# Kernel optimization log

Hardware: AMD Instinct MI355X
Metric: run time of the kernel (lower is better)

The kernel has to match this reference:

```python
import jax, jax.numpy as jnp
import numpy as np

B, N, F_IN, F_OUT = 128, 512, 128, 64
ALPHA = 0.2        # LeakyReLU slope for attention logits
GAIN = 1.414       # xavier gain used in the torch module
NEG_INF = -9e15    # mask value from the torch code


def _xavier_uniform(key, shape, gain):
    fan_in, fan_out = shape[0], shape[1]
    limit = gain * np.sqrt(6.0 / (fan_in + fan_out))
    return jax.random.uniform(key, shape, jnp.float32, -limit, limit)


def setup_inputs() -> dict:
    key = jax.random.key(0)
    k1, k2, k3, k4 = jax.random.split(key, 4)
    input_hid = jax.random.normal(k1, (B, N, F_IN), jnp.float32)
    adj = jax.random.randint(k2, (B, N, N), 0, 2, jnp.int32)  # 0/1 adjacency
    W = _xavier_uniform(k3, (F_IN, F_OUT), GAIN)
    a = _xavier_uniform(k4, (2 * F_OUT, 1), GAIN)
    return {"input_hid": input_hid, "adj": adj, "W": W, "a": a}


def reference(input_hid, adj, W, a):
    # h: [B, N, F_OUT]
    h = jnp.matmul(input_hid, W)
    # Standard GAT decomposition of the concat-repeat construction:
    # e[b,i,j] = leakyrelu( [h_i || h_j] @ a ) = leakyrelu( h_i@a_src + h_j@a_dst )
    a_src = a[:F_OUT, 0]   # applies to the repeated-row (i) half
    a_dst = a[F_OUT:, 0]   # applies to the tiled (j) half
    s = jnp.einsum('bnf,f->bn', h, a_src)  # [B, N]
    t = jnp.einsum('bnf,f->bn', h, a_dst)  # [B, N]
    e = jax.nn.leaky_relu(s[:, :, None] + t[:, None, :], ALPHA)  # [B, N, N]
    e = jnp.where(adj > 0, e, NEG_INF)
    att = jax.nn.softmax(e, axis=2)        # softmax over neighbors j
    h_prime = jnp.matmul(att, h)           # [B, N, F_OUT]
    # concat=True -> F.leaky_relu with torch default slope 0.01
    return jax.nn.leaky_relu(h_prime, 0.01)
```

## Files before the change

kernel.cpp:

```cpp
#include <hip/hip_runtime.h>
#include <stdint.h>

#define B_   128
#define N_   512
#define FIN  128
#define FOUT 64

using bf16x8 = __attribute__((ext_vector_type(8))) short;
using f32x4  = __attribute__((ext_vector_type(4))) float;

__device__ inline unsigned short f2bf(float x) {
    union { float f; uint32_t u; } c; c.f = x;
    uint32_t u = c.u;
    return (unsigned short)((u + 0x7FFFu + ((u >> 16) & 1u)) >> 16);
}

__global__ __launch_bounds__(256) void k_h(const float* __restrict__ X,
                                           const float* __restrict__ W,
                                           const float* __restrict__ a,
                                           uint16_t* __restrict__ htT,
                                           float* __restrict__ s,
                                           float* __restrict__ t) {
    __shared__ bf16x8 ax[32 * 64];
    __shared__ bf16x8 wl[16 * 64];

    const int b  = blockIdx.x >> 2;
    const int j0 = (blockIdx.x & 3) * 128;
    const int tid = threadIdx.x;
    const int w = tid >> 6, lane = tid & 63;
    const int q = lane >> 4, m = lane & 15;

#pragma unroll
    for (int nt = 0; nt < 4; ++nt) {
        bf16x8 fr;
#pragma unroll
        for (int u = 0; u < 8; ++u)
            fr[u] = (short)f2bf(W[(w * 32 + q * 8 + u) * FOUT + nt * 16 + m]);
        wl[(w * 4 + nt) * 64 + lane] = fr;
    }

    const float* xb = X + ((size_t)(b * N_) + j0) * FIN;
#pragma unroll
    for (int i = 0; i < 8; ++i) {
        int pi = i * 4 + w, rt = pi >> 2, ks = pi & 3;
        const float* src = xb + (size_t)(rt * 16 + m) * FIN + ks * 32 + q * 8;
        float4 v0 = *(const float4*)src;
        float4 v1 = *(const float4*)(src + 4);
        bf16x8 fr;
        fr[0] = (short)f2bf(v0.x); fr[1] = (short)f2bf(v0.y);
        fr[2] = (short)f2bf(v0.z); fr[3] = (short)f2bf(v0.w);
        fr[4] = (short)f2bf(v1.x); fr[5] = (short)f2bf(v1.y);
        fr[6] = (short)f2bf(v1.z); fr[7] = (short)f2bf(v1.w);
        ax[pi * 64 + lane] = fr;
    }
    __syncthreads();

    float asv[4], adv[4];
#pragma unroll
    for (int nt = 0; nt < 4; ++nt) {
        asv[nt] = a[nt * 16 + m];
        adv[nt] = a[FOUT + nt * 16 + m];
    }

    for (int rl = 0; rl < 2; ++rl) {
        const int rt = w + rl * 4;
        f32x4 acc[4] = {{0.f,0.f,0.f,0.f},{0.f,0.f,0.f,0.f},
                        {0.f,0.f,0.f,0.f},{0.f,0.f,0.f,0.f}};
#pragma unroll
        for (int ks = 0; ks < 4; ++ks) {
            bf16x8 af = ax[(rt * 4 + ks) * 64 + lane];
#pragma unroll
            for (int nt = 0; nt < 4; ++nt)
                acc[nt] = __builtin_amdgcn_mfma_f32_16x16x32_bf16(
                    af, wl[(ks * 4 + nt) * 64 + lane], acc[nt], 0, 0, 0);
        }

        float ps[4], pt[4];
#pragma unroll
        for (int r = 0; r < 4; ++r) {
            float vs = 0.f, vt = 0.f;
#pragma unroll
            for (int nt = 0; nt < 4; ++nt) {
                vs += acc[nt][r] * asv[nt];
                vt += acc[nt][r] * adv[nt];
            }
            vs += __shfl_xor(vs, 1, 64); vs += __shfl_xor(vs, 2, 64);
            vs += __shfl_xor(vs, 4, 64); vs += __shfl_xor(vs, 8, 64);
            vt += __shfl_xor(vt, 1, 64); vt += __shfl_xor(vt, 2, 64);
            vt += __shfl_xor(vt, 4, 64); vt += __shfl_xor(vt, 8, 64);
            ps[r] = vs; pt[r] = vt;
        }
        if (m < 4) {
            float vs = (m == 0) ? ps[0] : (m == 1) ? ps[1] : (m == 2) ? ps[2] : ps[3];
            float vt = (m == 0) ? pt[0] : (m == 1) ? pt[1] : (m == 2) ? pt[2] : pt[3];
            int row = j0 + rt * 16 + q * 4 + m;
            s[b * N_ + row] = vs;
            t[b * N_ + row] = vt;
        }

#pragma unroll
        for (int nt = 0; nt < 4; ++nt) {
            uint32_t d0 = (uint32_t)f2bf(acc[nt][0]) | ((uint32_t)f2bf(acc[nt][1]) << 16);
            uint32_t d1 = (uint32_t)f2bf(acc[nt][2]) | ((uint32_t)f2bf(acc[nt][3]) << 16);
            uint2 dd; dd.x = d0; dd.y = d1;
            *(uint2*)(htT + (size_t)(b * FOUT + nt * 16 + m) * N_ + j0 + rt * 16 + q * 4) = dd;
        }
    }
}

__global__ __launch_bounds__(256) void k_attn(const int*    __restrict__ adj,
                                              const uint16_t* __restrict__ htT,
                                              const float*  __restrict__ s,
                                              const float*  __restrict__ t,
                                              float*        __restrict__ out) {
    __shared__ bf16x8 hstage[64 * 64];

    const int b  = blockIdx.x >> 2;
    const int i0 = (blockIdx.x & 3) * 128;
    const int tid = threadIdx.x;
    const int w = tid >> 6, lane = tid & 63;
    const int q = lane >> 4, m = lane & 15;

    const uint16_t* hb = htT + (size_t)b * FOUT * N_;
#pragma unroll
    for (int i = 0; i < 16; ++i) {
        int pi = i * 4 + w, ks = pi >> 2, nt = pi & 3;
        bf16x8 v = *(const bf16x8*)(hb + (size_t)(nt * 16 + m) * N_ + ks * 32 + q * 8);
        hstage[pi * 64 + lane] = v;
    }
    __syncthreads();

    const float* tb = t + b * N_;

    for (int rl = 0; rl < 2; ++rl) {
        const int rt = w + rl * 4;
        const int irow = i0 + rt * 16 + m;
        const float s_i = s[b * N_ + irow];
        const int* adjrow = adj + ((size_t)(b * N_) + irow) * N_;

        f32x4 acc0 = {0.f,0.f,0.f,0.f}, acc1 = {0.f,0.f,0.f,0.f};
        f32x4 acc2 = {0.f,0.f,0.f,0.f}, acc3 = {0.f,0.f,0.f,0.f};
        float lsum = 0.f;

        for (int ks = 0; ks < 16; ++ks) {
            const int jb = ks * 32 + q * 8;
            float4 t0 = *(const float4*)(tb + jb);
            float4 t1 = *(const float4*)(tb + jb + 4);
            int4  a0 = *(const int4*)(adjrow + jb);
            int4  a1 = *(const int4*)(adjrow + jb + 4);

            float tj[8] = {t0.x, t0.y, t0.z, t0.w, t1.x, t1.y, t1.z, t1.w};
            int   av[8] = {a0.x, a0.y, a0.z, a0.w, a1.x, a1.y, a1.z, a1.w};
            float pv[8];
#pragma unroll
            for (int u = 0; u < 8; ++u) {
                float e = s_i + tj[u];
                e = fmaxf(e, 0.2f * e);
                pv[u] = (av[u] > 0) ? __expf(e) : 0.0f;
                lsum += pv[u];
            }
            bf16x8 af;
#pragma unroll
            for (int u = 0; u < 8; ++u) af[u] = (short)f2bf(pv[u]);

            bf16x8 b0 = hstage[(ks * 4 + 0) * 64 + lane];
            bf16x8 b1 = hstage[(ks * 4 + 1) * 64 + lane];
            bf16x8 b2 = hstage[(ks * 4 + 2) * 64 + lane];
            bf16x8 b3 = hstage[(ks * 4 + 3) * 64 + lane];

            acc0 = __builtin_amdgcn_mfma_f32_16x16x32_bf16(af, b0, acc0, 0, 0, 0);
            acc1 = __builtin_amdgcn_mfma_f32_16x16x32_bf16(af, b1, acc1, 0, 0, 0);
            acc2 = __builtin_amdgcn_mfma_f32_16x16x32_bf16(af, b2, acc2, 0, 0, 0);
            acc3 = __builtin_amdgcn_mfma_f32_16x16x32_bf16(af, b3, acc3, 0, 0, 0);
        }

        lsum += __shfl_xor(lsum, 16, 64);
        lsum += __shfl_xor(lsum, 32, 64);

#pragma unroll
        for (int reg = 0; reg < 4; ++reg) {
            float lr = __shfl(lsum, q * 4 + reg, 64);
            float inv = 1.0f / lr;
            int orow = i0 + rt * 16 + q * 4 + reg;
            size_t obase = ((size_t)(b * N_) + orow) * FOUT + m;
            float v0 = acc0[reg] * inv; v0 = fmaxf(v0, 0.01f * v0);
            float v1 = acc1[reg] * inv; v1 = fmaxf(v1, 0.01f * v1);
            float v2 = acc2[reg] * inv; v2 = fmaxf(v2, 0.01f * v2);
            float v3 = acc3[reg] * inv; v3 = fmaxf(v3, 0.01f * v3);
            out[obase +  0] = v0;
            out[obase + 16] = v1;
            out[obase + 32] = v2;
            out[obase + 48] = v3;
        }
    }
}

extern "C" void kernel_launch(void* const* d_in, const int* in_sizes, int n_in,
                              void* d_out, int out_size, void* d_ws, size_t ws_size,
                              hipStream_t stream) {
    const float* X   = (const float*)d_in[0];
    const int*   adj = (const int*)  d_in[1];
    const float* W   = (const float*)d_in[2];
    const float* a   = (const float*)d_in[3];
    float* out = (float*)d_out;

    uint16_t* htT = (uint16_t*)d_ws;
    float* s = (float*)(htT + (size_t)B_ * FOUT * N_);
    float* t = s + B_ * N_;

    k_h<<<B_ * 4, 256, 0, stream>>>(X, W, a, htT, s, t);
    k_attn<<<B_ * 4, 256, 0, stream>>>(adj, htT, s, t, out);
}
```

Before: 232.3 us.

## Process both row tiles together, prefetch adjacency, stage t in LDS

The attention kernel now handles its two 16-row tiles in a single fused loop instead of two sequential passes. It software-prefetches the next adjacency chunk one iteration ahead and stages the t vector in shared memory rather than reloading it from global memory each step. The aim is more memory-level parallelism on the dominant adjacency stream and shared B-fragment loads across both tiles. The cost is higher register pressure from doubled accumulators and prefetch registers, which may reduce occupancy.

```diff
diff --git a/kernel.cpp b/kernel.cpp
--- a/kernel.cpp
+++ b/kernel.cpp
@@ -114,6 +114,7 @@
                                               const float*  __restrict__ t,
                                               float*        __restrict__ out) {
     __shared__ bf16x8 hstage[64 * 64];
+    __shared__ float  tsh[N_];
 
     const int b  = blockIdx.x >> 2;
     const int i0 = (blockIdx.x & 3) * 128;
@@ -128,69 +129,92 @@
         bf16x8 v = *(const bf16x8*)(hb + (size_t)(nt * 16 + m) * N_ + ks * 32 + q * 8);
         hstage[pi * 64 + lane] = v;
     }
+    *(float2*)&tsh[tid * 2] = *(const float2*)(t + b * N_ + tid * 2);
     __syncthreads();
 
-    const float* tb = t + b * N_;
-
-    for (int rl = 0; rl < 2; ++rl) {
-        const int rt = w + rl * 4;
-        const int irow = i0 + rt * 16 + m;
-        const float s_i = s[b * N_ + irow];
-        const int* adjrow = adj + ((size_t)(b * N_) + irow) * N_;
-
-        f32x4 acc0 = {0.f,0.f,0.f,0.f}, acc1 = {0.f,0.f,0.f,0.f};
-        f32x4 acc2 = {0.f,0.f,0.f,0.f}, acc3 = {0.f,0.f,0.f,0.f};
-        float lsum = 0.f;
-
-        for (int ks = 0; ks < 16; ++ks) {
-            const int jb = ks * 32 + q * 8;
-            float4 t0 = *(const float4*)(tb + jb);
-            float4 t1 = *(const float4*)(tb + jb + 4);
-            int4  a0 = *(const int4*)(adjrow + jb);
-            int4  a1 = *(const int4*)(adjrow + jb + 4);
-
-            float tj[8] = {t0.x, t0.y, t0.z, t0.w, t1.x, t1.y, t1.z, t1.w};
-            int   av[8] = {a0.x, a0.y, a0.z, a0.w, a1.x, a1.y, a1.z, a1.w};
-            float pv[8];
-#pragma unroll
-            for (int u = 0; u < 8; ++u) {
-                float e = s_i + tj[u];
-                e = fmaxf(e, 0.2f * e);
-                pv[u] = (av[u] > 0) ? __expf(e) : 0.0f;
-                lsum += pv[u];
-            }
-            bf16x8 af;
-#pragma unroll
-            for (int u = 0; u < 8; ++u) af[u] = (short)f2bf(pv[u]);
-
-            bf16x8 b0 = hstage[(ks * 4 + 0) * 64 + lane];
-            bf16x8 b1 = hstage[(ks * 4 + 1) * 64 + lane];
-            bf16x8 b2 = hstage[(ks * 4 + 2) * 64 + lane];
-            bf16x8 b3 = hstage[(ks * 4 + 3) * 64 + lane];
-
-            acc0 = __builtin_amdgcn_mfma_f32_16x16x32_bf16(af, b0, acc0, 0, 0, 0);
-            acc1 = __builtin_amdgcn_mfma_f32_16x16x32_bf16(af, b1, acc1, 0, 0, 0);
-            acc2 = __builtin_amdgcn_mfma_f32_16x16x32_bf16(af, b2, acc2, 0, 0, 0);
-            acc3 = __builtin_amdgcn_mfma_f32_16x16x32_bf16(af, b3, acc3, 0, 0, 0);
-        }
-
-        lsum += __shfl_xor(lsum, 16, 64);
-        lsum += __shfl_xor(lsum, 32, 64);
-
-#pragma unroll
-        for (int reg = 0; reg < 4; ++reg) {
-            float lr = __shfl(lsum, q * 4 + reg, 64);
-            float inv = 1.0f / lr;
-            int orow = i0 + rt * 16 + q * 4 + reg;
-            size_t obase = ((size_t)(b * N_) + orow) * FOUT + m;
-            float v0 = acc0[reg] * inv; v0 = fmaxf(v0, 0.01f * v0);
-            float v1 = acc1[reg] * inv; v1 = fmaxf(v1, 0.01f * v1);
-            float v2 = acc2[reg] * inv; v2 = fmaxf(v2, 0.01f * v2);
-            float v3 = acc3[reg] * inv; v3 = fmaxf(v3, 0.01f * v3);
-            out[obase +  0] = v0;
-            out[obase + 16] = v1;
-            out[obase + 32] = v2;
-            out[obase + 48] = v3;
+    const int ir0 = i0 + w * 16 + m;
+    const int ir1 = ir0 + 64;
+    const float s0 = s[b * N_ + ir0];
+    const float s1 = s[b * N_ + ir1];
+    const int* ar0 = adj + ((size_t)(b * N_) + ir0) * N_;
+    const int* ar1 = adj + ((size_t)(b * N_) + ir1) * N_;
+
+    f32x4 acc0[4] = {{0.f,0.f,0.f,0.f},{0.f,0.f,0.f,0.f},
+                     {0.f,0.f,0.f,0.f},{0.f,0.f,0.f,0.f}};
+    f32x4 acc1[4] = {{0.f,0.f,0.f,0.f},{0.f,0.f,0.f,0.f},
+                     {0.f,0.f,0.f,0.f},{0.f,0.f,0.f,0.f}};
+    float ls0 = 0.f, ls1 = 0.f;
+
+    int4 c00 = *(const int4*)(ar0 + q * 8);
+    int4 c01 = *(const int4*)(ar0 + q * 8 + 4);
+    int4 c10 = *(const int4*)(ar1 + q * 8);
+    int4 c11 = *(const int4*)(ar1 + q * 8 + 4);
+
+    for (int ks = 0; ks < 16; ++ks) {
+        const int jn = ((ks < 15) ? ks + 1 : ks) * 32 + q * 8;
+        int4 n00 = *(const int4*)(ar0 + jn);
+        int4 n01 = *(const int4*)(ar0 + jn + 4);
+        int4 n10 = *(const int4*)(ar1 + jn);
+        int4 n11 = *(const int4*)(ar1 + jn + 4);
+
+        const int jb = ks * 32 + q * 8;
+        float tj[8];
+#pragma unroll
+        for (int u = 0; u < 8; ++u) tj[u] = tsh[jb + u];
+
+        int av0[8] = {c00.x, c00.y, c00.z, c00.w, c01.x, c01.y, c01.z, c01.w};
+        int av1[8] = {c10.x, c10.y, c10.z, c10.w, c11.x, c11.y, c11.z, c11.w};
+        bf16x8 af0, af1;
+#pragma unroll
+        for (int u = 0; u < 8; ++u) {
+            float e0 = s0 + tj[u];
+            e0 = fmaxf(e0, 0.2f * e0);
+            float p0 = (av0[u] > 0) ? __expf(e0) : 0.0f;
+            ls0 += p0;
+            af0[u] = (short)f2bf(p0);
+            float e1 = s1 + tj[u];
+            e1 = fmaxf(e1, 0.2f * e1);
+            float p1 = (av1[u] > 0) ? __expf(e1) : 0.0f;
+            ls1 += p1;
+            af1[u] = (short)f2bf(p1);
+        }
+
+        bf16x8 bf0 = hstage[(ks * 4 + 0) * 64 + lane];
+        bf16x8 bf1 = hstage[(ks * 4 + 1) * 64 + lane];
+        bf16x8 bf2 = hstage[(ks * 4 + 2) * 64 + lane];
+        bf16x8 bf3 = hstage[(ks * 4 + 3) * 64 + lane];
+
+        acc0[0] = __builtin_amdgcn_mfma_f32_16x16x32_bf16(af0, bf0, acc0[0], 0, 0, 0);
+        acc0[1] = __builtin_amdgcn_mfma_f32_16x16x32_bf16(af0, bf1, acc0[1], 0, 0, 0);
+        acc0[2] = __builtin_amdgcn_mfma_f32_16x16x32_bf16(af0, bf2, acc0[2], 0, 0, 0);
+        acc0[3] = __builtin_amdgcn_mfma_f32_16x16x32_bf16(af0, bf3, acc0[3], 0, 0, 0);
+        acc1[0] = __builtin_amdgcn_mfma_f32_16x16x32_bf16(af1, bf0, acc1[0], 0, 0, 0);
+        acc1[1] = __builtin_amdgcn_mfma_f32_16x16x32_bf16(af1, bf1, acc1[1], 0, 0, 0);
+        acc1[2] = __builtin_amdgcn_mfma_f32_16x16x32_bf16(af1, bf2, acc1[2], 0, 0, 0);
+        acc1[3] = __builtin_amdgcn_mfma_f32_16x16x32_bf16(af1, bf3, acc1[3], 0, 0, 0);
+
+        c00 = n00; c01 = n01; c10 = n10; c11 = n11;
+    }
+
+    ls0 += __shfl_xor(ls0, 16, 64);
+    ls0 += __shfl_xor(ls0, 32, 64);
+    ls1 += __shfl_xor(ls1, 16, 64);
+    ls1 += __shfl_xor(ls1, 32, 64);
+
+#pragma unroll
+    for (int reg = 0; reg < 4; ++reg) {
+        float lr0 = __shfl(ls0, q * 4 + reg, 64);
+        float lr1 = __shfl(ls1, q * 4 + reg, 64);
+        float inv0 = 1.0f / lr0, inv1 = 1.0f / lr1;
+        int orow0 = i0 + w * 16 + q * 4 + reg;
+        size_t ob0 = ((size_t)(b * N_) + orow0) * FOUT + m;
+        size_t ob1 = ob0 + (size_t)64 * FOUT;
+#pragma unroll
+        for (int nt = 0; nt < 4; ++nt) {
+            float v0 = acc0[nt][reg] * inv0; v0 = fmaxf(v0, 0.01f * v0);
+            float v1 = acc1[nt][reg] * inv1; v1 = fmaxf(v1, 0.01f * v1);
+            out[ob0 + nt * 16] = v0;
+            out[ob1 + nt * 16] = v1;
         }
     }
 }
```

New measurement: 231.7 us. Within noise of the previous version (-0.3%).

## Shrink attention tiles, halve LDS staging, prefetch adjacency, load X directly

Applied to the files above, without the earlier changes.

The attention kernel now gives each block 64 rows instead of 128 and launches twice as many blocks. It stages the bf16 h matrix in two halves so LDS drops to half, caches t in shared memory, and prefetches the next adjacency chunk one step ahead. The h kernel drops its LDS staging of X and converts the X rows to bf16 straight from global memory in the MFMA loop. The aim is more occupancy and better hiding of the dominant int32 adjacency stream. In exchange, each block now re-stages h and adds an extra sync pair mid-loop.

```diff
diff --git a/kernel.cpp b/kernel.cpp
--- a/kernel.cpp
+++ b/kernel.cpp
@@ -21,7 +21,6 @@
                                            uint16_t* __restrict__ htT,
                                            float* __restrict__ s,
                                            float* __restrict__ t) {
-    __shared__ bf16x8 ax[32 * 64];
     __shared__ bf16x8 wl[16 * 64];
 
     const int b  = blockIdx.x >> 2;
@@ -38,21 +37,6 @@
             fr[u] = (short)f2bf(W[(w * 32 + q * 8 + u) * FOUT + nt * 16 + m]);
         wl[(w * 4 + nt) * 64 + lane] = fr;
     }
-
-    const float* xb = X + ((size_t)(b * N_) + j0) * FIN;
-#pragma unroll
-    for (int i = 0; i < 8; ++i) {
-        int pi = i * 4 + w, rt = pi >> 2, ks = pi & 3;
-        const float* src = xb + (size_t)(rt * 16 + m) * FIN + ks * 32 + q * 8;
-        float4 v0 = *(const float4*)src;
-        float4 v1 = *(const float4*)(src + 4);
-        bf16x8 fr;
-        fr[0] = (short)f2bf(v0.x); fr[1] = (short)f2bf(v0.y);
-        fr[2] = (short)f2bf(v0.z); fr[3] = (short)f2bf(v0.w);
-        fr[4] = (short)f2bf(v1.x); fr[5] = (short)f2bf(v1.y);
-        fr[6] = (short)f2bf(v1.z); fr[7] = (short)f2bf(v1.w);
-        ax[pi * 64 + lane] = fr;
-    }
     __syncthreads();
 
     float asv[4], adv[4];
@@ -62,13 +46,22 @@
         adv[nt] = a[FOUT + nt * 16 + m];
     }
 
+    const float* xb = X + ((size_t)(b * N_) + j0) * FIN;
+
     for (int rl = 0; rl < 2; ++rl) {
         const int rt = w + rl * 4;
+        const float* xrow = xb + (size_t)(rt * 16 + m) * FIN + q * 8;
         f32x4 acc[4] = {{0.f,0.f,0.f,0.f},{0.f,0.f,0.f,0.f},
                         {0.f,0.f,0.f,0.f},{0.f,0.f,0.f,0.f}};
 #pragma unroll
         for (int ks = 0; ks < 4; ++ks) {
-            bf16x8 af = ax[(rt * 4 + ks) * 64 + lane];
+            float4 v0 = *(const float4*)(xrow + ks * 32);
+            float4 v1 = *(const float4*)(xrow + ks * 32 + 4);
+            bf16x8 af;
+            af[0] = (short)f2bf(v0.x); af[1] = (short)f2bf(v0.y);
+            af[2] = (short)f2bf(v0.z); af[3] = (short)f2bf(v0.w);
+            af[4] = (short)f2bf(v1.x); af[5] = (short)f2bf(v1.y);
+            af[6] = (short)f2bf(v1.z); af[7] = (short)f2bf(v1.w);
 #pragma unroll
             for (int nt = 0; nt < 4; ++nt)
                 acc[nt] = __builtin_amdgcn_mfma_f32_16x16x32_bf16(
@@ -108,49 +101,56 @@
     }
 }
 
-__global__ __launch_bounds__(256) void k_attn(const int*    __restrict__ adj,
-                                              const uint16_t* __restrict__ htT,
-                                              const float*  __restrict__ s,
-                                              const float*  __restrict__ t,
-                                              float*        __restrict__ out) {
-    __shared__ bf16x8 hstage[64 * 64];
-
-    const int b  = blockIdx.x >> 2;
-    const int i0 = (blockIdx.x & 3) * 128;
+__global__ __launch_bounds__(256, 4) void k_attn(const int*    __restrict__ adj,
+                                                 const uint16_t* __restrict__ htT,
+                                                 const float*  __restrict__ s,
+                                                 const float*  __restrict__ t,
+                                                 float*        __restrict__ out) {
+    __shared__ bf16x8 hstage[32 * 64];
+    __shared__ float  tsh[N_];
+
+    const int b  = blockIdx.x >> 3;
+    const int i0 = (blockIdx.x & 7) * 64;
     const int tid = threadIdx.x;
     const int w = tid >> 6, lane = tid & 63;
     const int q = lane >> 4, m = lane & 15;
 
     const uint16_t* hb = htT + (size_t)b * FOUT * N_;
-#pragma unroll
-    for (int i = 0; i < 16; ++i) {
+
+#pragma unroll
+    for (int i = 0; i < 8; ++i) {
         int pi = i * 4 + w, ks = pi >> 2, nt = pi & 3;
-        bf16x8 v = *(const bf16x8*)(hb + (size_t)(nt * 16 + m) * N_ + ks * 32 + q * 8);
-        hstage[pi * 64 + lane] = v;
-    }
+        hstage[pi * 64 + lane] =
+            *(const bf16x8*)(hb + (size_t)(nt * 16 + m) * N_ + ks * 32 + q * 8);
+    }
+    *(float2*)&tsh[tid * 2] = *(const float2*)(t + b * N_ + tid * 2);
     __syncthreads();
 
-    const float* tb = t + b * N_;
-
-    for (int rl = 0; rl < 2; ++rl) {
-        const int rt = w + rl * 4;
-        const int irow = i0 + rt * 16 + m;
-        const float s_i = s[b * N_ + irow];
-        const int* adjrow = adj + ((size_t)(b * N_) + irow) * N_;
-
-        f32x4 acc0 = {0.f,0.f,0.f,0.f}, acc1 = {0.f,0.f,0.f,0.f};
-        f32x4 acc2 = {0.f,0.f,0.f,0.f}, acc3 = {0.f,0.f,0.f,0.f};
-        float lsum = 0.f;
-
-        for (int ks = 0; ks < 16; ++ks) {
+    const int irow = i0 + w * 16 + m;
+    const float s_i = s[b * N_ + irow];
+    const int* ar = adj + ((size_t)(b * N_) + irow) * N_;
+
+    f32x4 acc[4] = {{0.f,0.f,0.f,0.f},{0.f,0.f,0.f,0.f},
+                    {0.f,0.f,0.f,0.f},{0.f,0.f,0.f,0.f}};
+    float lsum = 0.f;
+
+    int4 c0 = *(const int4*)(ar + q * 8);
+    int4 c1 = *(const int4*)(ar + q * 8 + 4);
+
+    for (int half = 0; half < 2; ++half) {
+        for (int kk = 0; kk < 8; ++kk) {
+            const int ks = half * 8 + kk;
+            const int jn = ((ks < 15) ? ks + 1 : ks) * 32 + q * 8;
+            int4 n0 = *(const int4*)(ar + jn);
+            int4 n1 = *(const int4*)(ar + jn + 4);
+
             const int jb = ks * 32 + q * 8;
-            float4 t0 = *(const float4*)(tb + jb);
-            float4 t1 = *(const float4*)(tb + jb + 4);
-            int4  a0 = *(const int4*)(adjrow + jb);
-            int4  a1 = *(const int4*)(adjrow + jb + 4);
-
-            float tj[8] = {t0.x, t0.y, t0.z, t0.w, t1.x, t1.y, t1.z, t1.w};
-            int   av[8] = {a0.x, a0.y, a0.z, a0.w, a1.x, a1.y, a1.z, a1.w};
+            float tj[8];
+#pragma unroll
+            for (int u = 0; u < 8; ++u) tj[u] = tsh[jb + u];
+
+            int av[8] = {c0.x, c0.y, c0.z, c0.w, c1.x, c1.y, c1.z, c1.w};
+            bf16x8 af;
             float pv[8];
 #pragma unroll
             for (int u = 0; u < 8; ++u) {
@@ -158,39 +158,47 @@
                 e = fmaxf(e, 0.2f * e);
                 pv[u] = (av[u] > 0) ? __expf(e) : 0.0f;
                 lsum += pv[u];
+                af[u] = (short)f2bf(pv[u]);
             }
-            bf16x8 af;
-#pragma unroll
-            for (int u = 0; u < 8; ++u) af[u] = (short)f2bf(pv[u]);
-
-            bf16x8 b0 = hstage[(ks * 4 + 0) * 64 + lane];
-            bf16x8 b1 = hstage[(ks * 4 + 1) * 64 + lane];
-            bf16x8 b2 = hstage[(ks * 4 + 2) * 64 + lane];
-            bf16x8 b3 = hstage[(ks * 4 + 3) * 64 + lane];
-
-            acc0 = __builtin_amdgcn_mfma_f32_16x16x32_bf16(af, b0, acc0, 0, 0, 0);
-            acc1 = __builtin_amdgcn_mfma_f32_16x16x32_bf16(af, b1, acc1, 0, 0, 0);
-            acc2 = __builtin_amdgcn_mfma_f32_16x16x32_bf16(af, b2, acc2, 0, 0, 0);
-            acc3 = __builtin_amdgcn_mfma_f32_16x16x32_bf16(af, b3, acc3, 0, 0, 0);
-        }
-
-        lsum += __shfl_xor(lsum, 16, 64);
-        lsum += __shfl_xor(lsum, 32, 64);
-
-#pragma unroll
-        for (int reg = 0; reg < 4; ++reg) {
-            float lr = __shfl(lsum, q * 4 + reg, 64);
-            float inv = 1.0f / lr;
-            int orow = i0 + rt * 16 + q * 4 + reg;
-            size_t obase = ((size_t)(b * N_) + orow) * FOUT + m;
-            float v0 = acc0[reg] * inv; v0 = fmaxf(v0, 0.01f * v0);
-            float v1 = acc1[reg] * inv; v1 = fmaxf(v1, 0.01f * v1);
-            float v2 = acc2[reg] * inv; v2 = fmaxf(v2, 0.01f * v2);
-            float v3 = acc3[reg] * inv; v3 = fmaxf(v3, 0.01f * v3);
-            out[obase +  0] = v0;
-            out[obase + 16] = v1;
-            out[obase + 32] = v2;
-            out[obase + 48] = v3;
+
+            bf16x8 bf0 = hstage[(kk * 4 + 0) * 64 + lane];
+            bf16x8 bf1 = hstage[(kk * 4 + 1) * 64 + lane];
+            bf16x8 bf2 = hstage[(kk * 4 + 2) * 64 + lane];
+            bf16x8 bf3 = hstage[(kk * 4 + 3) * 64 + lane];
+
+            acc[0] = __builtin_amdgcn_mfma_f32_16x16x32_bf16(af, bf0, acc[0], 0, 0, 0);
+            acc[1] = __builtin_amdgcn_mfma_f32_16x16x32_bf16(af, bf1, acc[1], 0, 0, 0);
+            acc[2] = __builtin_amdgcn_mfma_f32_16x16x32_bf16(af, bf2, acc[2], 0, 0, 0);
+            acc[3] = __builtin_amdgcn_mfma_f32_16x16x32_bf16(af, bf3, acc[3], 0, 0, 0);
+
+            c0 = n0; c1 = n1;
+        }
+        if (half == 0) {
+            __syncthreads();
+#pragma unroll
+            for (int i = 0; i < 8; ++i) {
+                int pi = i * 4 + w, ks = 8 + (pi >> 2), nt = pi & 3;
+                hstage[pi * 64 + lane] =
+                    *(const bf16x8*)(hb + (size_t)(nt * 16 + m) * N_ + ks * 32 + q * 8);
+            }
+            __syncthreads();
+        }
+    }
+
+    lsum += __shfl_xor(lsum, 16, 64);
+    lsum += __shfl_xor(lsum, 32, 64);
+
+#pragma unroll
+    for (int reg = 0; reg < 4; ++reg) {
+        float lr = __shfl(lsum, q * 4 + reg, 64);
+        float inv = 1.0f / lr;
+        int orow = i0 + w * 16 + q * 4 + reg;
+        size_t ob = ((size_t)(b * N_) + orow) * FOUT + m;
+#pragma unroll
+        for (int nt = 0; nt < 4; ++nt) {
+            float v = acc[nt][reg] * inv;
+            v = fmaxf(v, 0.01f * v);
+            out[ob + nt * 16] = v;
         }
     }
 }
@@ -209,5 +217,5 @@
     float* t = s + B_ * N_;
 
     k_h<<<B_ * 4, 256, 0, stream>>>(X, W, a, htT, s, t);
-    k_attn<<<B_ * 4, 256, 0, stream>>>(adj, htT, s, t, out);
-}
+    k_attn<<<B_ * 8, 256, 0, stream>>>(adj, htT, s, t, out);
+}
```

After: 245.9 us. +5.9%, slower.
